# Kernel tuning notes

Hardware: AMD Instinct MI355X
Metric: run time of the kernel (lower is better)

## Reference

```python
import jax, jax.numpy as jnp
import numpy as np

HID, OUT, EMB, NL = 256, 128, 1024, 4
NR, NP_, NM = 16384, 40000, 30000
E = 200000
NTYPES = 3  # lin_nodes keys: protein, molecule, reaction


def setup_inputs() -> dict:
    key = jax.random.key(0)
    ks = jax.random.split(key, 32)
    f32 = jnp.float32
    inp = {}
    inp["x_reaction"] = jax.random.normal(ks[0], (NR, EMB), f32)
    inp["x_protein"] = jax.random.normal(ks[1], (NP_, EMB), f32)
    inp["x_molecule"] = jax.random.normal(ks[2], (NM, EMB), f32)
    inp["ei_p2r_src"] = jax.random.randint(ks[3], (E,), 0, NP_, jnp.int32)
    inp["ei_p2r_dst"] = jax.random.randint(ks[4], (E,), 0, NR, jnp.int32)
    inp["ei_m2r_src"] = jax.random.randint(ks[5], (E,), 0, NM, jnp.int32)
    inp["ei_m2r_dst"] = jax.random.randint(ks[6], (E,), 0, NR, jnp.int32)
    inp["ei_r2p_src"] = jax.random.randint(ks[7], (E,), 0, NR, jnp.int32)
    inp["ei_r2p_dst"] = jax.random.randint(ks[8], (E,), 0, NP_, jnp.int32)
    inp["ei_r2m_src"] = jax.random.randint(ks[9], (E,), 0, NR, jnp.int32)
    inp["ei_r2m_dst"] = jax.random.randint(ks[10], (E,), 0, NM, jnp.int32)
    inp["output_notes_opt"] = jax.random.normal(ks[11], (NR, EMB), f32)
    inp["output_types"] = jax.random.randint(ks[12], (NR,), 0, NTYPES, jnp.int32)
    s = 0.02
    # layer 0 SAGE params (lazy in_dim = EMB), one set per edge type (4 edge types)
    inp["Wl0"] = jax.random.normal(ks[13], (4, EMB, HID), f32) * s
    inp["Wr0"] = jax.random.normal(ks[14], (4, EMB, HID), f32) * s
    inp["bl0"] = jnp.zeros((4, HID), f32)
    # layers 1..3 SAGE params (in_dim = HID)
    inp["Wl"] = jax.random.normal(ks[15], (NL - 1, 4, HID, HID), f32) * s
    inp["Wr"] = jax.random.normal(ks[16], (NL - 1, 4, HID, HID), f32) * s
    inp["bl"] = jnp.zeros((NL - 1, 4, HID), f32)
    inp["W_reaction"] = jax.random.normal(ks[17], (HID, OUT), f32) * s
    inp["b_reaction"] = jnp.zeros((OUT,), f32)
    inp["W_nodes"] = jax.random.normal(ks[18], (NTYPES, EMB, OUT), f32) * s
    inp["b_nodes"] = jnp.zeros((NTYPES, OUT), f32)
    return inp


def _sage(x_src, x_dst, src, dst, n_dst, Wl, bl, Wr):
    # PyG SAGEConv (aggr='mean'): lin_l(mean_{j->i} x_j) + lin_r(x_i); lin_l has bias.
    g = x_src[src]                                              # [E, d] gather
    s = jax.ops.segment_sum(g, dst, num_segments=n_dst)          # [n_dst, d]
    cnt = jax.ops.segment_sum(jnp.ones((src.shape[0],), x_src.dtype), dst, num_segments=n_dst)
    mean = s / jnp.maximum(cnt, 1.0)[:, None]
    return mean @ Wl + bl + x_dst @ Wr


def _hetero_layer(xr, xp, xm, edges, Wl, bl, Wr):
    # HeteroConv(aggr='sum'): sum SAGE outputs per destination node type.
    (ps, pd), (ms, md), (rps, rpd), (rms, rmd) = edges
    new_r = (_sage(xp, xr, ps, pd, NR, Wl[0], bl[0], Wr[0])
             + _sage(xm, xr, ms, md, NR, Wl[1], bl[1], Wr[1]))
    new_p = _sage(xr, xp, rps, rpd, NP_, Wl[2], bl[2], Wr[2])
    new_m = _sage(xr, xm, rms, rmd, NM, Wl[3], bl[3], Wr[3])
    return new_r, new_p, new_m


def reference(x_reaction, x_protein, x_molecule,
              ei_p2r_src, ei_p2r_dst, ei_m2r_src, ei_m2r_dst,
              ei_r2p_src, ei_r2p_dst, ei_r2m_src, ei_r2m_dst,
              output_notes_opt, output_types,
              Wl0, bl0, Wr0, Wl, bl, Wr,
              W_reaction, b_reaction, W_nodes, b_nodes):
    edges = ((ei_p2r_src, ei_p2r_dst), (ei_m2r_src, ei_m2r_dst),
             (ei_r2p_src, ei_r2p_dst), (ei_r2m_src, ei_r2m_dst))
    xr, xp, xm = _hetero_layer(x_reaction, x_protein, x_molecule, edges, Wl0, bl0, Wr0)
    for l in range(NL - 1):
        xr, xp, xm = _hetero_layer(xr, xp, xm, edges, Wl[l], bl[l], Wr[l])
    reaction_out = xr @ W_reaction + b_reaction                  # [NR, OUT]
    # lin_nodes[t](v) per output node: project with all type linears, select by type id
    projs = jnp.einsum('ke,ted->ktd', output_notes_opt, W_nodes) + b_nodes[None]  # [NR, T, OUT]
    node_out = jnp.take_along_axis(projs, output_types[:, None, None].astype(jnp.int32), axis=1)[:, 0, :]
    # cosine similarity along dim=1, torch-style eps clamp on the norm product
    num = jnp.sum(reaction_out * node_out, axis=-1)
    den = jnp.maximum(jnp.linalg.norm(reaction_out, axis=-1) * jnp.linalg.norm(node_out, axis=-1), 1e-8)
    return (num / den + 1.0) * 0.5
```

## Files before the change

### kernel.cpp

```cpp
#include <hip/hip_runtime.h>
#include <math.h>
#include <stdint.h>

#define NR_ 16384
#define NP2_ 40000
#define NM_ 30000
#define NE_ 200000
#define EMB_ 1024
#define HID_ 256
#define OUTD_ 128

typedef __attribute__((ext_vector_type(8))) short bf16x8;
typedef __attribute__((ext_vector_type(4))) float f32x4;
typedef __attribute__((ext_vector_type(8))) unsigned short us8;

__device__ __forceinline__ unsigned short f2bf(float f) {
    uint32_t u = __builtin_bit_cast(uint32_t, f);
    u = (u + 0x7FFFu + ((u >> 16) & 1u)) >> 16;
    return (unsigned short)u;
}
__device__ __forceinline__ float bf2f(unsigned short u) {
    uint32_t v = ((uint32_t)u) << 16;
    return __builtin_bit_cast(float, v);
}

struct Csr4 {
    const int* src[4]; const int* dst[4];
    int* offs[4]; int* cur[4]; int* csr[4];
    int n[4];
};
__global__ void k_zero4(Csr4 c) {
    int y = blockIdx.y;
    int i = blockIdx.x * 256 + threadIdx.x;
    if (i < c.n[y]) c.cur[y][i] = 0;
}
__global__ void k_deg4(Csr4 c) {
    int y = blockIdx.y;
    int i = blockIdx.x * 256 + threadIdx.x;
    if (i < NE_) atomicAdd(&c.cur[y][c.dst[y][i]], 1);
}
__global__ void k_scanA(Csr4 c, int* __restrict__ csum) {
    int y = blockIdx.y;
    int n = c.n[y];
    int ch = blockIdx.x;
    int nch = (n + 1023) >> 10;
    if (ch >= nch) return;
    const int* deg = c.cur[y];
    int* offs = c.offs[y];
    __shared__ int ts[256];
    int base = ch << 10;
    int t = threadIdx.x;
    int v[4];
    int s = 0;
    #pragma unroll
    for (int k = 0; k < 4; ++k) {
        int i = base + t * 4 + k;
        v[k] = (i < n) ? deg[i] : 0;
        s += v[k];
    }
    ts[t] = s;
    __syncthreads();
    for (int st = 1; st < 256; st <<= 1) {
        int x = ts[t];
        int xo = (t >= st) ? ts[t - st] : 0;
        __syncthreads();
        ts[t] = x + xo;
        __syncthreads();
    }
    int run = (t > 0) ? ts[t - 1] : 0;
    #pragma unroll
    for (int k = 0; k < 4; ++k) {
        int i = base + t * 4 + k;
        if (i < n) offs[i] = run;
        run += v[k];
    }
    if (t == 255) csum[y * 40 + ch] = ts[255];
}
__global__ void k_scanB(Csr4 c, int* __restrict__ csum) {
    int y = threadIdx.x;
    if (y < 4) {
        int n = c.n[y];
        int nch = (n + 1023) >> 10;
        int acc = 0;
        for (int i = 0; i < nch; ++i) {
            int v = csum[y * 40 + i];
            csum[y * 40 + i] = acc;
            acc += v;
        }
        c.offs[y][n] = acc;
    }
}
__global__ void k_scanC(Csr4 c, const int* __restrict__ csum) {
    int y = blockIdx.y;
    int i = blockIdx.x * 256 + threadIdx.x;
    if (i < c.n[y]) {
        int v = c.offs[y][i] + csum[y * 40 + (i >> 10)];
        c.offs[y][i] = v;
        c.cur[y][i] = v;
    }
}
__global__ void k_scatter4(Csr4 c) {
    int y = blockIdx.y;
    int i = blockIdx.x * 256 + threadIdx.x;
    if (i < NE_) {
        int d = c.dst[y][i];
        int p = atomicAdd(&c.cur[y][d], 1);
        c.csr[y][p] = c.src[y][i];
    }
}

struct WItem { const float* a; const float* b; unsigned short* dst; int k; int n; };
struct WBatch { WItem it[32]; };
__global__ void k_wconvT(WBatch wb) {
    WItem w = wb.it[blockIdx.y];
    int total = w.k * w.n;
    int kmask = w.k - 1;
    int shift = (w.k == 1024) ? 10 : 8;
    for (int idx = blockIdx.x * 256 + threadIdx.x; idx < total; idx += gridDim.x * 256) {
        int k = idx & kmask, n = idx >> shift;
        float v = w.a[(size_t)k * w.n + n];
        if (w.b) v += w.b[(size_t)k * w.n + n];
        w.dst[idx] = f2bf(v);
    }
}

struct GSeg {
    const void* A; const unsigned short* Bt; void* C; const float* bias;
    int lda, ldc, M, K, ntn, blk0, af32;
};
struct GBatch { GSeg s[3]; int b1, b2, tot; };

template <bool OBF, bool AF32>
__global__ __launch_bounds__(256, 4) void k_gemmb(GBatch gb) {
    __shared__ __align__(16) unsigned short As[128 * 64];
    __shared__ __align__(16) unsigned short Bs[128 * 64];
    const int tid = threadIdx.x;
    const int lane = tid & 63;
    int nwg = gb.tot;
    int o = blockIdx.x;
    int q = nwg >> 3, r = nwg & 7;
    int xcd = o & 7, j = o >> 3;
    int wg = (xcd < r ? xcd * (q + 1) : r * (q + 1) + (xcd - r) * q) + j;
    const int si = (wg >= gb.b1) + (wg >= gb.b2);
    const GSeg sg = gb.s[si];
    const int local = wg - sg.blk0;
    const int bm = (local / sg.ntn) * 128;
    const int bn = (local % sg.ntn) * 128;
    const int lda = sg.lda, ldc = sg.ldc, M = sg.M, K = sg.K;
    const unsigned short* __restrict__ Bt = sg.Bt;
    const float* __restrict__ bias = sg.bias;

    const int wave = tid >> 6;
    const int wr = (wave >> 1) * 64;
    const int wc = (wave & 1) * 64;
    const int frow = lane & 15;
    const int fkc = lane >> 4;
    f32x4 acc[4][4] = {};

    for (int k0 = 0; k0 < K; k0 += 64) {
        #pragma unroll
        for (int i = 0; i < 4; ++i) {
            int c = tid + i * 256;
            int row = c >> 3, kc = c & 7;
            int srck = k0 + ((kc ^ (row & 7)) << 3);
            int ga = min(bm + row, M - 1);
            if constexpr (AF32) {
                const float* Af = (const float*)sg.A + (size_t)ga * lda + srck;
                float4 a0 = *(const float4*)Af;
                float4 a1 = *(const float4*)(Af + 4);
                us8 oo;
                oo[0] = f2bf(a0.x); oo[1] = f2bf(a0.y); oo[2] = f2bf(a0.z); oo[3] = f2bf(a0.w);
                oo[4] = f2bf(a1.x); oo[5] = f2bf(a1.y); oo[6] = f2bf(a1.z); oo[7] = f2bf(a1.w);
                *(us8*)(As + (size_t)c * 8) = oo;
            } else {
                __builtin_amdgcn_global_load_lds(
                    (const __attribute__((address_space(1))) unsigned int*)((const unsigned short*)sg.A + (size_t)ga * lda + srck),
                    (__attribute__((address_space(3))) unsigned int*)(As + (size_t)c * 8), 16, 0, 0);
            }
            __builtin_amdgcn_global_load_lds(
                (const __attribute__((address_space(1))) unsigned int*)(Bt + (size_t)(bn + row) * K + srck),
                (__attribute__((address_space(3))) unsigned int*)(Bs + (size_t)c * 8), 16, 0, 0);
        }
        __syncthreads();
        #pragma unroll
        for (int kk = 0; kk < 2; ++kk) {
            bf16x8 af[4], bfr[4];
            #pragma unroll
            for (int m = 0; m < 4; ++m) {
                int row = wr + m * 16 + frow;
                int kc = kk * 4 + fkc;
                af[m] = *(const bf16x8*)(As + (size_t)((row << 3) + (kc ^ (row & 7))) * 8);
            }
            #pragma unroll
            for (int n = 0; n < 4; ++n) {
                int row = wc + n * 16 + frow;
                int kc = kk * 4 + fkc;
                bfr[n] = *(const bf16x8*)(Bs + (size_t)((row << 3) + (kc ^ (row & 7))) * 8);
            }
            #pragma unroll
            for (int m = 0; m < 4; ++m)
                #pragma unroll
                for (int n = 0; n < 4; ++n)
                    acc[m][n] = __builtin_amdgcn_mfma_f32_16x16x32_bf16(bfr[n], af[m], acc[m][n], 0, 0, 0);
        }
        __syncthreads();
    }

    const int ccol0 = (lane >> 4) << 2;
    #pragma unroll
    for (int m = 0; m < 4; ++m) {
        int row = bm + wr + m * 16 + frow;
        if (row < M) {
            #pragma unroll
            for (int n = 0; n < 4; ++n) {
                int col = bn + wc + n * 16 + ccol0;
                f32x4 v = acc[m][n];
                if (bias) {
                    v[0] += bias[col + 0];
                    v[1] += bias[col + 1];
                    v[2] += bias[col + 2];
                    v[3] += bias[col + 3];
                }
                if constexpr (OBF) {
                    ushort4 oo;
                    oo.x = f2bf(v[0]); oo.y = f2bf(v[1]); oo.z = f2bf(v[2]); oo.w = f2bf(v[3]);
                    *(ushort4*)((unsigned short*)sg.C + (size_t)row * ldc + col) = oo;
                } else {
                    *(float4*)((float*)sg.C + (size_t)row * ldc + col) = make_float4(v[0], v[1], v[2], v[3]);
                }
            }
        }
    }
}

__global__ __launch_bounds__(256, 4) void k_gemmf(GBatch gb) {
    __shared__ __align__(16) unsigned short As[128 * 64];
    __shared__ __align__(16) unsigned short Bs[128 * 64];
    const int tid = threadIdx.x;
    const int lane = tid & 63;
    int nwg = gb.tot;
    int o = blockIdx.x;
    int q = nwg >> 3, r = nwg & 7;
    int xcd = o & 7, j = o >> 3;
    int wg = (xcd < r ? xcd * (q + 1) : r * (q + 1) + (xcd - r) * q) + j;
    const int si = (wg >= gb.b1) + (wg >= gb.b2);
    const GSeg sg = gb.s[si];
    const int local = wg - sg.blk0;
    const int bm = (local / sg.ntn) * 128;
    const int bn = (local % sg.ntn) * 128;
    const int lda = sg.lda, ldc = sg.ldc, M = sg.M, K = sg.K;
    const unsigned short* __restrict__ Bt = sg.Bt;
    const float* __restrict__ bias = sg.bias;

    const int wave = tid >> 6;
    const int wr = (wave >> 1) * 64;
    const int wc = (wave & 1) * 64;
    const int frow = lane & 15;
    const int fkc = lane >> 4;
    f32x4 acc[4][4] = {};

    for (int k0 = 0; k0 < K; k0 += 64) {
        #pragma unroll
        for (int i = 0; i < 4; ++i) {
            int c = tid + i * 256;
            int row = c >> 3, kc = c & 7;
            int srck = k0 + ((kc ^ (row & 7)) << 3);
            int ga = min(bm + row, M - 1);
            if (sg.af32) {
                const float* Af = (const float*)sg.A + (size_t)ga * lda + srck;
                float4 a0 = *(const float4*)Af;
                float4 a1 = *(const float4*)(Af + 4);
                us8 oo;
                oo[0] = f2bf(a0.x); oo[1] = f2bf(a0.y); oo[2] = f2bf(a0.z); oo[3] = f2bf(a0.w);
                oo[4] = f2bf(a1.x); oo[5] = f2bf(a1.y); oo[6] = f2bf(a1.z); oo[7] = f2bf(a1.w);
                *(us8*)(As + (size_t)c * 8) = oo;
            } else {
                __builtin_amdgcn_global_load_lds(
                    (const __attribute__((address_space(1))) unsigned int*)((const unsigned short*)sg.A + (size_t)ga * lda + srck),
                    (__attribute__((address_space(3))) unsigned int*)(As + (size_t)c * 8), 16, 0, 0);
            }
            __builtin_amdgcn_global_load_lds(
                (const __attribute__((address_space(1))) unsigned int*)(Bt + (size_t)(bn + row) * K + srck),
                (__attribute__((address_space(3))) unsigned int*)(Bs + (size_t)c * 8), 16, 0, 0);
        }
        __syncthreads();
        #pragma unroll
        for (int kk = 0; kk < 2; ++kk) {
            bf16x8 af[4], bfr[4];
            #pragma unroll
            for (int m = 0; m < 4; ++m) {
                int row = wr + m * 16 + frow;
                int kc = kk * 4 + fkc;
                af[m] = *(const bf16x8*)(As + (size_t)((row << 3) + (kc ^ (row & 7))) * 8);
            }
            #pragma unroll
            for (int n = 0; n < 4; ++n) {
                int row = wc + n * 16 + frow;
                int kc = kk * 4 + fkc;
                bfr[n] = *(const bf16x8*)(Bs + (size_t)((row << 3) + (kc ^ (row & 7))) * 8);
            }
            #pragma unroll
            for (int m = 0; m < 4; ++m)
                #pragma unroll
                for (int n = 0; n < 4; ++n)
                    acc[m][n] = __builtin_amdgcn_mfma_f32_16x16x32_bf16(bfr[n], af[m], acc[m][n], 0, 0, 0);
        }
        __syncthreads();
    }

    const int ccol0 = (lane >> 4) << 2;
    #pragma unroll
    for (int m = 0; m < 4; ++m) {
        int row = bm + wr + m * 16 + frow;
        if (row < M) {
            #pragma unroll
            for (int n = 0; n < 4; ++n) {
                int col = bn + wc + n * 16 + ccol0;
                f32x4 v = acc[m][n];
                v[0] += bias[col + 0];
                v[1] += bias[col + 1];
                v[2] += bias[col + 2];
                v[3] += bias[col + 3];
                *(float4*)((float*)sg.C + (size_t)row * ldc + col) = make_float4(v[0], v[1], v[2], v[3]);
            }
        }
    }
}

struct ASeg {
    const int* offsA; const int* csrA; const unsigned short* projA; int ldpA; const float* biasA;
    const int* offsB; const int* csrB; const unsigned short* projB; int ldpB; const float* biasB;
    unsigned short* outx; int ldo; int ndst; int blk0;
};
struct ABatch { ASeg s[3]; int b1, b2; };

__global__ __launch_bounds__(256) void k_aggb(ABatch ab) {
    int b = blockIdx.x;
    int si = (b >= ab.b1) + (b >= ab.b2);
    const ASeg sg = ab.s[si];
    int node = (b - sg.blk0) * 4 + (threadIdx.x >> 6);
    int lane = threadIdx.x & 63;
    if (node >= sg.ndst) return;

    float a0 = 0.f, a1 = 0.f, a2 = 0.f, a3 = 0.f;
    int begA = sg.offsA[node], endA = sg.offsA[node + 1];
    {
        const unsigned short* baseA = sg.projA + lane * 4;
        const int* csrA = sg.csrA;
        int ldpA = sg.ldpA;
        int e = begA;
        for (; e + 3 < endA; e += 4) {
            int i0 = csrA[e], i1 = csrA[e + 1], i2 = csrA[e + 2], i3 = csrA[e + 3];
            ushort4 u0 = *(const ushort4*)(baseA + (size_t)i0 * ldpA);
            ushort4 u1 = *(const ushort4*)(baseA + (size_t)i1 * ldpA);
            ushort4 u2 = *(const ushort4*)(baseA + (size_t)i2 * ldpA);
            ushort4 u3 = *(const ushort4*)(baseA + (size_t)i3 * ldpA);
            a0 += bf2f(u0.x) + bf2f(u1.x) + bf2f(u2.x) + bf2f(u3.x);
            a1 += bf2f(u0.y) + bf2f(u1.y) + bf2f(u2.y) + bf2f(u3.y);
            a2 += bf2f(u0.z) + bf2f(u1.z) + bf2f(u2.z) + bf2f(u3.z);
            a3 += bf2f(u0.w) + bf2f(u1.w) + bf2f(u2.w) + bf2f(u3.w);
        }
        for (; e < endA; ++e) {
            ushort4 u = *(const ushort4*)(baseA + (size_t)csrA[e] * ldpA);
            a0 += bf2f(u.x); a1 += bf2f(u.y); a2 += bf2f(u.z); a3 += bf2f(u.w);
        }
    }
    float invA = 1.f / fmaxf((float)(endA - begA), 1.f);
    float4 bA = ((const float4*)sg.biasA)[lane];
    float r0 = a0 * invA + bA.x;
    float r1 = a1 * invA + bA.y;
    float r2 = a2 * invA + bA.z;
    float r3 = a3 * invA + bA.w;

    if (sg.csrB) {
        float b0 = 0.f, b1 = 0.f, b2 = 0.f, b3 = 0.f;
        int begB = sg.offsB[node], endB = sg.offsB[node + 1];
        const unsigned short* baseB = sg.projB + lane * 4;
        const int* csrB = sg.csrB;
        int ldpB = sg.ldpB;
        int e = begB;
        for (; e + 3 < endB; e += 4) {
            int i0 = csrB[e], i1 = csrB[e + 1], i2 = csrB[e + 2], i3 = csrB[e + 3];
            ushort4 u0 = *(const ushort4*)(baseB + (size_t)i0 * ldpB);
            ushort4 u1 = *(const ushort4*)(baseB + (size_t)i1 * ldpB);
            ushort4 u2 = *(const ushort4*)(baseB + (size_t)i2 * ldpB);
            ushort4 u3 = *(const ushort4*)(baseB + (size_t)i3 * ldpB);
            b0 += bf2f(u0.x) + bf2f(u1.x) + bf2f(u2.x) + bf2f(u3.x);
            b1 += bf2f(u0.y) + bf2f(u1.y) + bf2f(u2.y) + bf2f(u3.y);
            b2 += bf2f(u0.z) + bf2f(u1.z) + bf2f(u2.z) + bf2f(u3.z);
            b3 += bf2f(u0.w) + bf2f(u1.w) + bf2f(u2.w) + bf2f(u3.w);
        }
        for (; e < endB; ++e) {
            ushort4 u = *(const ushort4*)(baseB + (size_t)csrB[e] * ldpB);
            b0 += bf2f(u.x); b1 += bf2f(u.y); b2 += bf2f(u.z); b3 += bf2f(u.w);
        }
        float invB = 1.f / fmaxf((float)(endB - begB), 1.f);
        float4 bB = ((const float4*)sg.biasB)[lane];
        r0 += b0 * invB + bB.x;
        r1 += b1 * invB + bB.y;
        r2 += b2 * invB + bB.z;
        r3 += b3 * invB + bB.w;
    }

    size_t o = (size_t)node * sg.ldo + lane * 4;
    ushort4 cur = *(const ushort4*)(sg.outx + o);
    ushort4 w;
    w.x = f2bf(bf2f(cur.x) + r0);
    w.y = f2bf(bf2f(cur.y) + r1);
    w.z = f2bf(bf2f(cur.z) + r2);
    w.w = f2bf(bf2f(cur.w) + r3);
    *(ushort4*)(sg.outx + o) = w;
}

__global__ __launch_bounds__(256) void k_cos(const float* __restrict__ ro,
                                             const float* __restrict__ pr,
                                             const int* __restrict__ types,
                                             float* __restrict__ out, int nr) {
    int row = blockIdx.x * 4 + (threadIdx.x >> 6);
    int lane = threadIdx.x & 63;
    if (row >= nr) return;
    int t = types[row];
    float2 r = ((const float2*)(ro + (size_t)row * OUTD_))[lane];
    float2 nn = ((const float2*)(pr + (size_t)row * 384 + t * OUTD_))[lane];
    float num = r.x * nn.x + r.y * nn.y;
    float d1 = r.x * r.x + r.y * r.y;
    float d2 = nn.x * nn.x + nn.y * nn.y;
    #pragma unroll
    for (int s = 1; s < 64; s <<= 1) {
        num += __shfl_xor(num, s);
        d1 += __shfl_xor(d1, s);
        d2 += __shfl_xor(d2, s);
    }
    if (lane == 0) out[row] = (num / fmaxf(sqrtf(d1) * sqrtf(d2), 1e-8f) + 1.f) * 0.5f;
}

extern "C" void kernel_launch(void* const* d_in, const int* in_sizes, int n_in,
                              void* d_out, int out_size, void* d_ws, size_t ws_size,
                              hipStream_t stream) {
    const float* x_r0 = (const float*)d_in[0];
    const float* x_p0 = (const float*)d_in[1];
    const float* x_m0 = (const float*)d_in[2];
    const int* e_src[4] = {(const int*)d_in[3], (const int*)d_in[5], (const int*)d_in[7], (const int*)d_in[9]};
    const int* e_dst[4] = {(const int*)d_in[4], (const int*)d_in[6], (const int*)d_in[8], (const int*)d_in[10]};
    const float* notes = (const float*)d_in[11];
    const int* types = (const int*)d_in[12];
    const float* Wl0 = (const float*)d_in[13];
    const float* Wr0 = (const float*)d_in[14];
    const float* bl0 = (const float*)d_in[15];
    const float* WlL = (const float*)d_in[16];
    const float* WrL = (const float*)d_in[17];
    const float* blL = (const float*)d_in[18];
    const float* Wre = (const float*)d_in[19];
    const float* bre = (const float*)d_in[20];
    const float* Wn  = (const float*)d_in[21];
    const float* bn  = (const float*)d_in[22];
    float* out = (float*)d_out;

    uintptr_t base = (uintptr_t)d_ws;
    auto alloc = [&](size_t bytes) -> void* {
        uintptr_t p = (base + 255) & ~(uintptr_t)255;
        base = p + bytes;
        return (void*)p;
    };
    unsigned short* Rb[2] = {(unsigned short*)alloc((size_t)NR_ * 768 * 2),
                             (unsigned short*)alloc((size_t)NR_ * 768 * 2)};
    unsigned short* Pb[2] = {(unsigned short*)alloc((size_t)NP2_ * 512 * 2),
                             (unsigned short*)alloc((size_t)NP2_ * 512 * 2)};
    unsigned short* Mb[2] = {(unsigned short*)alloc((size_t)NM_ * 512 * 2),
                             (unsigned short*)alloc((size_t)NM_ * 512 * 2)};
    float* ro = (float*)alloc((size_t)NR_ * OUTD_ * 4);
    float* pr = (float*)alloc((size_t)NR_ * 384 * 4);
    unsigned short* wbf = (unsigned short*)alloc((size_t)4000000 * 2);
    int* csum = (int*)alloc(160 * 4);
    int nd[4] = {NR_, NR_, NP2_, NM_};
    Csr4 cs{};
    for (int t = 0; t < 4; ++t) {
        cs.src[t] = e_src[t]; cs.dst[t] = e_dst[t]; cs.n[t] = nd[t];
        cs.offs[t] = (int*)alloc(((size_t)nd[t] + 1) * 4);
        cs.cur[t]  = (int*)alloc((size_t)nd[t] * 4);
        cs.csr[t]  = (int*)alloc((size_t)NE_ * 4);
    }

    unsigned short *BR[4], *BP[4], *BM[4], *Bre, *Bn;
    {
        WBatch wb{};
        int cnt = 0;
        size_t woff = 0;
        auto add = [&](const float* a, const float* bb, int K, int N) -> unsigned short* {
            unsigned short* dst = wbf + woff;
            woff += (size_t)K * N;
            wb.it[cnt] = WItem{a, bb, dst, K, N};
            ++cnt;
            return dst;
        };
        const size_t w0 = (size_t)EMB_ * HID_;
        const size_t wl = (size_t)HID_ * HID_;
        for (int l = 0; l < 4; ++l) {
            int K = (l == 0) ? EMB_ : HID_;
            const float* Wr_ = (l == 0) ? Wr0 : WrL + (size_t)(l - 1) * 4 * wl;
            const float* Wl_ = (l == 0) ? Wl0 : WlL + (size_t)(l - 1) * 4 * wl;
            size_t ws_ = (l == 0) ? w0 : wl;
            BR[l] = add(Wr_ + 0 * ws_, Wr_ + 1 * ws_, K, HID_);
            add(Wl_ + 2 * ws_, nullptr, K, HID_);
            add(Wl_ + 3 * ws_, nullptr, K, HID_);
            BP[l] = add(Wr_ + 2 * ws_, nullptr, K, HID_);
            add(Wl_ + 0 * ws_, nullptr, K, HID_);
            BM[l] = add(Wr_ + 3 * ws_, nullptr, K, HID_);
            add(Wl_ + 1 * ws_, nullptr, K, HID_);
        }
        Bre = add(Wre, nullptr, HID_, OUTD_);
        Bn = add(Wn + 0 * (size_t)EMB_ * OUTD_, nullptr, EMB_, OUTD_);
        add(Wn + 1 * (size_t)EMB_ * OUTD_, nullptr, EMB_, OUTD_);
        add(Wn + 2 * (size_t)EMB_ * OUTD_, nullptr, EMB_, OUTD_);
        k_wconvT<<<dim3(128, cnt), 256, 0, stream>>>(wb);
    }

    k_zero4<<<dim3((NP2_ + 255) / 256, 4), 256, 0, stream>>>(cs);
    k_deg4<<<dim3((NE_ + 255) / 256, 4), 256, 0, stream>>>(cs);
    k_scanA<<<dim3(40, 4), 256, 0, stream>>>(cs, csum);
    k_scanB<<<1, 64, 0, stream>>>(cs, csum);
    k_scanC<<<dim3((NP2_ + 255) / 256, 4), 256, 0, stream>>>(cs, csum);
    k_scatter4<<<dim3((NE_ + 255) / 256, 4), 256, 0, stream>>>(cs);

    const int MT_R = (NR_ + 127) / 128;
    const int MT_P = (NP2_ + 127) / 128;
    const int MT_M = (NM_ + 127) / 128;
    auto seg = [](const void* A, const unsigned short* Bt, void* C, const float* bias,
                  int lda, int ldc, int M, int K, int ntn, int blk0, int af32) -> GSeg {
        return GSeg{A, Bt, C, bias, lda, ldc, M, K, ntn, blk0, af32};
    };

    const int AB_R = (NR_ + 3) / 4, AB_P = (NP2_ + 3) / 4, AB_M = (NM_ + 3) / 4;

    for (int l = 0; l < 4; ++l) {
        int K = (l == 0) ? EMB_ : HID_;
        unsigned short* R = Rb[l & 1];
        unsigned short* P = Pb[l & 1];
        unsigned short* M = Mb[l & 1];
        const float* bl_ = (l == 0) ? bl0 : blL + (size_t)(l - 1) * 4 * HID_;

        GBatch gb{};
        int nR = MT_R * 6, nP = MT_P * 4, nM = MT_M * 4;
        if (l == 0) {
            gb.s[0] = seg(x_r0, BR[0], R, nullptr, EMB_, 768, NR_, EMB_, 6, 0, 1);
            gb.s[1] = seg(x_p0, BP[0], P, nullptr, EMB_, 512, NP2_, EMB_, 4, nR, 1);
            gb.s[2] = seg(x_m0, BM[0], M, nullptr, EMB_, 512, NM_, EMB_, 4, nR + nP, 1);
        } else {
            gb.s[0] = seg(Rb[(l - 1) & 1], BR[l], R, nullptr, 768, 768, NR_, K, 6, 0, 0);
            gb.s[1] = seg(Pb[(l - 1) & 1], BP[l], P, nullptr, 512, 512, NP2_, K, 4, nR, 0);
            gb.s[2] = seg(Mb[(l - 1) & 1], BM[l], M, nullptr, 512, 512, NM_, K, 4, nR + nP, 0);
        }
        gb.b1 = nR; gb.b2 = nR + nP; gb.tot = nR + nP + nM;
        if (l == 0) k_gemmb<true, true><<<gb.tot, 256, 0, stream>>>(gb);
        else        k_gemmb<true, false><<<gb.tot, 256, 0, stream>>>(gb);

        ABatch ab{};
        ab.s[0] = ASeg{cs.offs[0], cs.csr[0], P + 256, 512, bl_ + 0 * HID_,
                       cs.offs[1], cs.csr[1], M + 256, 512, bl_ + 1 * HID_,
                       R, 768, NR_, 0};
        ab.s[1] = ASeg{cs.offs[2], cs.csr[2], R + 256, 768, bl_ + 2 * HID_,
                       nullptr, nullptr, nullptr, 0, nullptr,
                       P, 512, NP2_, AB_R};
        ab.s[2] = ASeg{cs.offs[3], cs.csr[3], R + 512, 768, bl_ + 3 * HID_,
                       nullptr, nullptr, nullptr, 0, nullptr,
                       M, 512, NM_, AB_R + AB_P};
        ab.b1 = AB_R; ab.b2 = AB_R + AB_P;
        k_aggb<<<AB_R + AB_P + AB_M, 256, 0, stream>>>(ab);
    }

    {
        GBatch gf{};
        gf.s[0] = seg(Rb[1], Bre, ro, bre, 768, OUTD_, NR_, HID_, 1, 0, 0);
        gf.s[1] = seg(notes, Bn, pr, bn, EMB_, 384, NR_, EMB_, 3, MT_R, 1);
        gf.s[2] = gf.s[1];
        gf.b1 = MT_R; gf.b2 = MT_R + MT_R * 3; gf.tot = MT_R + MT_R * 3;
        k_gemmf<<<gf.tot, 256, 0, stream>>>(gf);
    }
    k_cos<<<NR_ / 4, 256, 0, stream>>>(ro, pr, types, out, NR_);
}
```

Before: 834.2 us.

## Add register-prefetch double-buffered GEMM for fp32-A inputs and split final GEMMs

Adds a new GEMM kernel for fp32 A operands that prefetches the next A tile into registers and double-buffers the B tile in shared memory, so global load latency overlaps with MFMA compute. It is used for the layer-0 and node-projection GEMMs. The mixed final GEMM is split into two launches (a bf16-A one and an fp32-A one), which removes the runtime af32 branch. Launch bounds drop from 4 to 3 waves per SIMD to leave room for the extra registers and LDS, at the cost of lower occupancy.

```diff
diff --git a/kernel.cpp b/kernel.cpp
--- a/kernel.cpp
+++ b/kernel.cpp
@@ -126,12 +126,12 @@
 
 struct GSeg {
     const void* A; const unsigned short* Bt; void* C; const float* bias;
-    int lda, ldc, M, K, ntn, blk0, af32;
+    int lda, ldc, M, K, ntn, blk0;
 };
 struct GBatch { GSeg s[3]; int b1, b2, tot; };
 
-template <bool OBF, bool AF32>
-__global__ __launch_bounds__(256, 4) void k_gemmb(GBatch gb) {
+template <bool OBF>
+__global__ __launch_bounds__(256, 3) void k_gemmb(GBatch gb) {
     __shared__ __align__(16) unsigned short As[128 * 64];
     __shared__ __align__(16) unsigned short Bs[128 * 64];
     const int tid = threadIdx.x;
@@ -164,19 +164,9 @@
             int row = c >> 3, kc = c & 7;
             int srck = k0 + ((kc ^ (row & 7)) << 3);
             int ga = min(bm + row, M - 1);
-            if constexpr (AF32) {
-                const float* Af = (const float*)sg.A + (size_t)ga * lda + srck;
-                float4 a0 = *(const float4*)Af;
-                float4 a1 = *(const float4*)(Af + 4);
-                us8 oo;
-                oo[0] = f2bf(a0.x); oo[1] = f2bf(a0.y); oo[2] = f2bf(a0.z); oo[3] = f2bf(a0.w);
-                oo[4] = f2bf(a1.x); oo[5] = f2bf(a1.y); oo[6] = f2bf(a1.z); oo[7] = f2bf(a1.w);
-                *(us8*)(As + (size_t)c * 8) = oo;
-            } else {
-                __builtin_amdgcn_global_load_lds(
-                    (const __attribute__((address_space(1))) unsigned int*)((const unsigned short*)sg.A + (size_t)ga * lda + srck),
-                    (__attribute__((address_space(3))) unsigned int*)(As + (size_t)c * 8), 16, 0, 0);
-            }
+            __builtin_amdgcn_global_load_lds(
+                (const __attribute__((address_space(1))) unsigned int*)((const unsigned short*)sg.A + (size_t)ga * lda + srck),
+                (__attribute__((address_space(3))) unsigned int*)(As + (size_t)c * 8), 16, 0, 0);
             __builtin_amdgcn_global_load_lds(
                 (const __attribute__((address_space(1))) unsigned int*)(Bt + (size_t)(bn + row) * K + srck),
                 (__attribute__((address_space(3))) unsigned int*)(Bs + (size_t)c * 8), 16, 0, 0);
@@ -233,9 +223,10 @@
     }
 }
 
-__global__ __launch_bounds__(256, 4) void k_gemmf(GBatch gb) {
+template <bool OBF>
+__global__ __launch_bounds__(256, 3) void k_gemma(GBatch gb) {
     __shared__ __align__(16) unsigned short As[128 * 64];
-    __shared__ __align__(16) unsigned short Bs[128 * 64];
+    __shared__ __align__(16) unsigned short Bs[2][128 * 64];
     const int tid = threadIdx.x;
     const int lane = tid & 63;
     int nwg = gb.tot;
@@ -258,55 +249,83 @@
     const int frow = lane & 15;
     const int fkc = lane >> 4;
     f32x4 acc[4][4] = {};
-
-    for (int k0 = 0; k0 < K; k0 += 64) {
-        #pragma unroll
-        for (int i = 0; i < 4; ++i) {
-            int c = tid + i * 256;
-            int row = c >> 3, kc = c & 7;
-            int srck = k0 + ((kc ^ (row & 7)) << 3);
-            int ga = min(bm + row, M - 1);
-            if (sg.af32) {
-                const float* Af = (const float*)sg.A + (size_t)ga * lda + srck;
-                float4 a0 = *(const float4*)Af;
-                float4 a1 = *(const float4*)(Af + 4);
-                us8 oo;
-                oo[0] = f2bf(a0.x); oo[1] = f2bf(a0.y); oo[2] = f2bf(a0.z); oo[3] = f2bf(a0.w);
-                oo[4] = f2bf(a1.x); oo[5] = f2bf(a1.y); oo[6] = f2bf(a1.z); oo[7] = f2bf(a1.w);
-                *(us8*)(As + (size_t)c * 8) = oo;
-            } else {
-                __builtin_amdgcn_global_load_lds(
-                    (const __attribute__((address_space(1))) unsigned int*)((const unsigned short*)sg.A + (size_t)ga * lda + srck),
-                    (__attribute__((address_space(3))) unsigned int*)(As + (size_t)c * 8), 16, 0, 0);
-            }
-            __builtin_amdgcn_global_load_lds(
-                (const __attribute__((address_space(1))) unsigned int*)(Bt + (size_t)(bn + row) * K + srck),
-                (__attribute__((address_space(3))) unsigned int*)(Bs + (size_t)c * 8), 16, 0, 0);
-        }
+    float4 ra0[4], ra1[4];
+
+#define ALOAD(kk0) do {                                                                    \
+    _Pragma("unroll")                                                                      \
+    for (int i = 0; i < 4; ++i) {                                                          \
+        int c = tid + i * 256, rw = c >> 3, kc = c & 7;                                    \
+        int srck = (kk0) + ((kc ^ (rw & 7)) << 3);                                         \
+        int ga = min(bm + rw, M - 1);                                                      \
+        const float* Af = (const float*)sg.A + (size_t)ga * lda + srck;                    \
+        ra0[i] = *(const float4*)Af;                                                       \
+        ra1[i] = *(const float4*)(Af + 4);                                                 \
+    } } while (0)
+
+#define AWRITE() do {                                                                      \
+    _Pragma("unroll")                                                                      \
+    for (int i = 0; i < 4; ++i) {                                                          \
+        int c = tid + i * 256;                                                             \
+        us8 oo;                                                                            \
+        oo[0] = f2bf(ra0[i].x); oo[1] = f2bf(ra0[i].y);                                    \
+        oo[2] = f2bf(ra0[i].z); oo[3] = f2bf(ra0[i].w);                                    \
+        oo[4] = f2bf(ra1[i].x); oo[5] = f2bf(ra1[i].y);                                    \
+        oo[6] = f2bf(ra1[i].z); oo[7] = f2bf(ra1[i].w);                                    \
+        *(us8*)(As + (size_t)c * 8) = oo;                                                  \
+    } } while (0)
+
+#define STAGE_B(bufi, kk0) do {                                                            \
+    _Pragma("unroll")                                                                      \
+    for (int i = 0; i < 4; ++i) {                                                          \
+        int c = tid + i * 256, rw = c >> 3, kc = c & 7;                                    \
+        int srck = (kk0) + ((kc ^ (rw & 7)) << 3);                                         \
+        __builtin_amdgcn_global_load_lds(                                                  \
+            (const __attribute__((address_space(1))) unsigned int*)(Bt + (size_t)(bn + rw) * K + srck), \
+            (__attribute__((address_space(3))) unsigned int*)(&Bs[bufi][(size_t)c * 8]), 16, 0, 0); \
+    } } while (0)
+
+#define COMPUTE(bufi) do {                                                                 \
+    _Pragma("unroll")                                                                      \
+    for (int kk = 0; kk < 2; ++kk) {                                                       \
+        bf16x8 af[4], bfr[4];                                                              \
+        _Pragma("unroll")                                                                  \
+        for (int m = 0; m < 4; ++m) {                                                      \
+            int rw = wr + m * 16 + frow;                                                   \
+            int kc = kk * 4 + fkc;                                                         \
+            af[m] = *(const bf16x8*)(As + (size_t)((rw << 3) + (kc ^ (rw & 7))) * 8);      \
+        }                                                                                  \
+        _Pragma("unroll")                                                                  \
+        for (int n = 0; n < 4; ++n) {                                                      \
+            int rw = wc + n * 16 + frow;                                                   \
+            int kc = kk * 4 + fkc;                                                         \
+            bfr[n] = *(const bf16x8*)(&Bs[bufi][(size_t)((rw << 3) + (kc ^ (rw & 7))) * 8]); \
+        }                                                                                  \
+        _Pragma("unroll")                                                                  \
+        for (int m = 0; m < 4; ++m)                                                        \
+            _Pragma("unroll")                                                              \
+            for (int n = 0; n < 4; ++n)                                                    \
+                acc[m][n] = __builtin_amdgcn_mfma_f32_16x16x32_bf16(bfr[n], af[m], acc[m][n], 0, 0, 0); \
+    } } while (0)
+
+    const int nt = K >> 6;
+    ALOAD(0);
+    STAGE_B(0, 0);
+    AWRITE();
+    __syncthreads();
+    for (int t = 0; t < nt; ++t) {
+        if (t + 1 < nt) {
+            ALOAD((t + 1) << 6);
+            STAGE_B((t + 1) & 1, (t + 1) << 6);
+        }
+        COMPUTE(t & 1);
         __syncthreads();
-        #pragma unroll
-        for (int kk = 0; kk < 2; ++kk) {
-            bf16x8 af[4], bfr[4];
-            #pragma unroll
-            for (int m = 0; m < 4; ++m) {
-                int row = wr + m * 16 + frow;
-                int kc = kk * 4 + fkc;
-                af[m] = *(const bf16x8*)(As + (size_t)((row << 3) + (kc ^ (row & 7))) * 8);
-            }
-            #pragma unroll
-            for (int n = 0; n < 4; ++n) {
-                int row = wc + n * 16 + frow;
-                int kc = kk * 4 + fkc;
-                bfr[n] = *(const bf16x8*)(Bs + (size_t)((row << 3) + (kc ^ (row & 7))) * 8);
-            }
-            #pragma unroll
-            for (int m = 0; m < 4; ++m)
-                #pragma unroll
-                for (int n = 0; n < 4; ++n)
-                    acc[m][n] = __builtin_amdgcn_mfma_f32_16x16x32_bf16(bfr[n], af[m], acc[m][n], 0, 0, 0);
-        }
+        if (t + 1 < nt) AWRITE();
         __syncthreads();
     }
+#undef ALOAD
+#undef AWRITE
+#undef STAGE_B
+#undef COMPUTE
 
     const int ccol0 = (lane >> 4) << 2;
     #pragma unroll
@@ -317,11 +336,19 @@
             for (int n = 0; n < 4; ++n) {
                 int col = bn + wc + n * 16 + ccol0;
                 f32x4 v = acc[m][n];
-                v[0] += bias[col + 0];
-                v[1] += bias[col + 1];
-                v[2] += bias[col + 2];
-                v[3] += bias[col + 3];
-                *(float4*)((float*)sg.C + (size_t)row * ldc + col) = make_float4(v[0], v[1], v[2], v[3]);
+                if (bias) {
+                    v[0] += bias[col + 0];
+                    v[1] += bias[col + 1];
+                    v[2] += bias[col + 2];
+                    v[3] += bias[col + 3];
+                }
+                if constexpr (OBF) {
+                    ushort4 oo;
+                    oo.x = f2bf(v[0]); oo.y = f2bf(v[1]); oo.z = f2bf(v[2]); oo.w = f2bf(v[3]);
+                    *(ushort4*)((unsigned short*)sg.C + (size_t)row * ldc + col) = oo;
+                } else {
+                    *(float4*)((float*)sg.C + (size_t)row * ldc + col) = make_float4(v[0], v[1], v[2], v[3]);
+                }
             }
         }
     }
@@ -526,8 +553,8 @@
     const int MT_P = (NP2_ + 127) / 128;
     const int MT_M = (NM_ + 127) / 128;
     auto seg = [](const void* A, const unsigned short* Bt, void* C, const float* bias,
-                  int lda, int ldc, int M, int K, int ntn, int blk0, int af32) -> GSeg {
-        return GSeg{A, Bt, C, bias, lda, ldc, M, K, ntn, blk0, af32};
+                  int lda, int ldc, int M, int K, int ntn, int blk0) -> GSeg {
+        return GSeg{A, Bt, C, bias, lda, ldc, M, K, ntn, blk0};
     };
 
     const int AB_R = (NR_ + 3) / 4, AB_P = (NP2_ + 3) / 4, AB_M = (NM_ + 3) / 4;
@@ -542,17 +569,17 @@
         GBatch gb{};
         int nR = MT_R * 6, nP = MT_P * 4, nM = MT_M * 4;
         if (l == 0) {
-            gb.s[0] = seg(x_r0, BR[0], R, nullptr, EMB_, 768, NR_, EMB_, 6, 0, 1);
-            gb.s[1] = seg(x_p0, BP[0], P, nullptr, EMB_, 512, NP2_, EMB_, 4, nR, 1);
-            gb.s[2] = seg(x_m0, BM[0], M, nullptr, EMB_, 512, NM_, EMB_, 4, nR + nP, 1);
+            gb.s[0] = seg(x_r0, BR[0], R, nullptr, EMB_, 768, NR_, EMB_, 6, 0);
+            gb.s[1] = seg(x_p0, BP[0], P, nullptr, EMB_, 512, NP2_, EMB_, 4, nR);
+            gb.s[2] = seg(x_m0, BM[0], M, nullptr, EMB_, 512, NM_, EMB_, 4, nR + nP);
         } else {
-            gb.s[0] = seg(Rb[(l - 1) & 1], BR[l], R, nullptr, 768, 768, NR_, K, 6, 0, 0);
-            gb.s[1] = seg(Pb[(l - 1) & 1], BP[l], P, nullptr, 512, 512, NP2_, K, 4, nR, 0);
-            gb.s[2] = seg(Mb[(l - 1) & 1], BM[l], M, nullptr, 512, 512, NM_, K, 4, nR + nP, 0);
+            gb.s[0] = seg(Rb[(l - 1) & 1], BR[l], R, nullptr, 768, 768, NR_, K, 6, 0);
+            gb.s[1] = seg(Pb[(l - 1) & 1], BP[l], P, nullptr, 512, 512, NP2_, K, 4, nR);
+            gb.s[2] = seg(Mb[(l - 1) & 1], BM[l], M, nullptr, 512, 512, NM_, K, 4, nR + nP);
         }
         gb.b1 = nR; gb.b2 = nR + nP; gb.tot = nR + nP + nM;
-        if (l == 0) k_gemmb<true, true><<<gb.tot, 256, 0, stream>>>(gb);
-        else        k_gemmb<true, false><<<gb.tot, 256, 0, stream>>>(gb);
+        if (l == 0) k_gemma<true><<<gb.tot, 256, 0, stream>>>(gb);
+        else        k_gemmb<true><<<gb.tot, 256, 0, stream>>>(gb);
 
         ABatch ab{};
         ab.s[0] = ASeg{cs.offs[0], cs.csr[0], P + 256, 512, bl_ + 0 * HID_,
@@ -569,12 +596,14 @@
     }
 
     {
-        GBatch gf{};
-        gf.s[0] = seg(Rb[1], Bre, ro, bre, 768, OUTD_, NR_, HID_, 1, 0, 0);
-        gf.s[1] = seg(notes, Bn, pr, bn, EMB_, 384, NR_, EMB_, 3, MT_R, 1);
-        gf.s[2] = gf.s[1];
-        gf.b1 = MT_R; gf.b2 = MT_R + MT_R * 3; gf.tot = MT_R + MT_R * 3;
-        k_gemmf<<<gf.tot, 256, 0, stream>>>(gf);
+        GBatch g1{};
+        g1.s[0] = seg(Rb[1], Bre, ro, bre, 768, OUTD_, NR_, HID_, 1, 0);
+        g1.b1 = g1.b2 = g1.tot = MT_R;
+        k_gemmb<false><<<g1.tot, 256, 0, stream>>>(g1);
+        GBatch g2{};
+        g2.s[0] = seg(notes, Bn, pr, bn, EMB_, 384, NR_, EMB_, 3, 0);
+        g2.b1 = g2.b2 = g2.tot = MT_R * 3;
+        k_gemma<false><<<g2.tot, 256, 0, stream>>>(g2);
     }
     k_cos<<<NR_ / 4, 256, 0, stream>>>(ro, pr, types, out, NR_);
 }
```

Measured after the change: 782.5 us. 6.2% less time.

## Enlarge GEMM tiles to 256x128 with 512-thread blocks and split final GEMM

Applied to the files above, without the earlier changes.

The batched GEMM kernel now computes 256-row by 128-column tiles using 512 threads (8 waves), doubling the A tile in LDS while sharing each B tile across twice as many rows. This cuts redundant loads of the weight tiles and halves the number of workgroups. The separate final-projection kernel is removed; the final projections now run as two launches of the templated kernel with compile-time A-format flags instead of a runtime branch. In exchange LDS use per block grows, which may lower occupancy, and the bigger tiles waste more work on partial tiles at the row edges.

```diff
diff --git a/kernel.cpp b/kernel.cpp
--- a/kernel.cpp
+++ b/kernel.cpp
@@ -126,13 +126,13 @@
 
 struct GSeg {
     const void* A; const unsigned short* Bt; void* C; const float* bias;
-    int lda, ldc, M, K, ntn, blk0, af32;
+    int lda, ldc, M, K, ntn, blk0;
 };
 struct GBatch { GSeg s[3]; int b1, b2, tot; };
 
 template <bool OBF, bool AF32>
-__global__ __launch_bounds__(256, 4) void k_gemmb(GBatch gb) {
-    __shared__ __align__(16) unsigned short As[128 * 64];
+__global__ __launch_bounds__(512, 6) void k_gemmb(GBatch gb) {
+    __shared__ __align__(16) unsigned short As[256 * 64];
     __shared__ __align__(16) unsigned short Bs[128 * 64];
     const int tid = threadIdx.x;
     const int lane = tid & 63;
@@ -144,7 +144,7 @@
     const int si = (wg >= gb.b1) + (wg >= gb.b2);
     const GSeg sg = gb.s[si];
     const int local = wg - sg.blk0;
-    const int bm = (local / sg.ntn) * 128;
+    const int bm = (local / sg.ntn) * 256;
     const int bn = (local % sg.ntn) * 128;
     const int lda = sg.lda, ldc = sg.ldc, M = sg.M, K = sg.K;
     const unsigned short* __restrict__ Bt = sg.Bt;
@@ -160,7 +160,7 @@
     for (int k0 = 0; k0 < K; k0 += 64) {
         #pragma unroll
         for (int i = 0; i < 4; ++i) {
-            int c = tid + i * 256;
+            int c = tid + i * 512;
             int row = c >> 3, kc = c & 7;
             int srck = k0 + ((kc ^ (row & 7)) << 3);
             int ga = min(bm + row, M - 1);
@@ -177,6 +177,12 @@
                     (const __attribute__((address_space(1))) unsigned int*)((const unsigned short*)sg.A + (size_t)ga * lda + srck),
                     (__attribute__((address_space(3))) unsigned int*)(As + (size_t)c * 8), 16, 0, 0);
             }
+        }
+        #pragma unroll
+        for (int i = 0; i < 2; ++i) {
+            int c = tid + i * 512;
+            int row = c >> 3, kc = c & 7;
+            int srck = k0 + ((kc ^ (row & 7)) << 3);
             __builtin_amdgcn_global_load_lds(
                 (const __attribute__((address_space(1))) unsigned int*)(Bt + (size_t)(bn + row) * K + srck),
                 (__attribute__((address_space(3))) unsigned int*)(Bs + (size_t)c * 8), 16, 0, 0);
@@ -228,100 +234,6 @@
                 } else {
                     *(float4*)((float*)sg.C + (size_t)row * ldc + col) = make_float4(v[0], v[1], v[2], v[3]);
                 }
-            }
-        }
-    }
-}
-
-__global__ __launch_bounds__(256, 4) void k_gemmf(GBatch gb) {
-    __shared__ __align__(16) unsigned short As[128 * 64];
-    __shared__ __align__(16) unsigned short Bs[128 * 64];
-    const int tid = threadIdx.x;
-    const int lane = tid & 63;
-    int nwg = gb.tot;
-    int o = blockIdx.x;
-    int q = nwg >> 3, r = nwg & 7;
-    int xcd = o & 7, j = o >> 3;
-    int wg = (xcd < r ? xcd * (q + 1) : r * (q + 1) + (xcd - r) * q) + j;
-    const int si = (wg >= gb.b1) + (wg >= gb.b2);
-    const GSeg sg = gb.s[si];
-    const int local = wg - sg.blk0;
-    const int bm = (local / sg.ntn) * 128;
-    const int bn = (local % sg.ntn) * 128;
-    const int lda = sg.lda, ldc = sg.ldc, M = sg.M, K = sg.K;
-    const unsigned short* __restrict__ Bt = sg.Bt;
-    const float* __restrict__ bias = sg.bias;
-
-    const int wave = tid >> 6;
-    const int wr = (wave >> 1) * 64;
-    const int wc = (wave & 1) * 64;
-    const int frow = lane & 15;
-    const int fkc = lane >> 4;
-    f32x4 acc[4][4] = {};
-
-    for (int k0 = 0; k0 < K; k0 += 64) {
-        #pragma unroll
-        for (int i = 0; i < 4; ++i) {
-            int c = tid + i * 256;
-            int row = c >> 3, kc = c & 7;
-            int srck = k0 + ((kc ^ (row & 7)) << 3);
-            int ga = min(bm + row, M - 1);
-            if (sg.af32) {
-                const float* Af = (const float*)sg.A + (size_t)ga * lda + srck;
-                float4 a0 = *(const float4*)Af;
-                float4 a1 = *(const float4*)(Af + 4);
-                us8 oo;
-                oo[0] = f2bf(a0.x); oo[1] = f2bf(a0.y); oo[2] = f2bf(a0.z); oo[3] = f2bf(a0.w);
-                oo[4] = f2bf(a1.x); oo[5] = f2bf(a1.y); oo[6] = f2bf(a1.z); oo[7] = f2bf(a1.w);
-                *(us8*)(As + (size_t)c * 8) = oo;
-            } else {
-                __builtin_amdgcn_global_load_lds(
-                    (const __attribute__((address_space(1))) unsigned int*)((const unsigned short*)sg.A + (size_t)ga * lda + srck),
-                    (__attribute__((address_space(3))) unsigned int*)(As + (size_t)c * 8), 16, 0, 0);
-            }
-            __builtin_amdgcn_global_load_lds(
-                (const __attribute__((address_space(1))) unsigned int*)(Bt + (size_t)(bn + row) * K + srck),
-                (__attribute__((address_space(3))) unsigned int*)(Bs + (size_t)c * 8), 16, 0, 0);
-        }
-        __syncthreads();
-        #pragma unroll
-        for (int kk = 0; kk < 2; ++kk) {
-            bf16x8 af[4], bfr[4];
-            #pragma unroll
-            for (int m = 0; m < 4; ++m) {
-                int row = wr + m * 16 + frow;
-                int kc = kk * 4 + fkc;
-                af[m] = *(const bf16x8*)(As + (size_t)((row << 3) + (kc ^ (row & 7))) * 8);
-            }
-            #pragma unroll
-            for (int n = 0; n < 4; ++n) {
-                int row = wc + n * 16 + frow;
-                int kc = kk * 4 + fkc;
-                bfr[n] = *(const bf16x8*)(Bs + (size_t)((row << 3) + (kc ^ (row & 7))) * 8);
-            }
-            #pragma unroll
-            for (int m = 0; m < 4; ++m)
-                #pragma unroll
-                for (int n = 0; n < 4; ++n)
-                    acc[m][n] = __builtin_amdgcn_mfma_f32_16x16x32_bf16(bfr[n], af[m], acc[m][n], 0, 0, 0);
-        }
-        __syncthreads();
-    }
-
-    const int ccol0 = (lane >> 4) << 2;
-    #pragma unroll
-    for (int m = 0; m < 4; ++m) {
-        int row = bm + wr + m * 16 + frow;
-        if (row < M) {
-            #pragma unroll
-            for (int n = 0; n < 4; ++n) {
-                int col = bn + wc + n * 16 + ccol0;
-                f32x4 v = acc[m][n];
-                v[0] += bias[col + 0];
-                v[1] += bias[col + 1];
-                v[2] += bias[col + 2];
-                v[3] += bias[col + 3];
-                *(float4*)((float*)sg.C + (size_t)row * ldc + col) = make_float4(v[0], v[1], v[2], v[3]);
             }
         }
     }
@@ -522,12 +434,12 @@
     k_scanC<<<dim3((NP2_ + 255) / 256, 4), 256, 0, stream>>>(cs, csum);
     k_scatter4<<<dim3((NE_ + 255) / 256, 4), 256, 0, stream>>>(cs);
 
-    const int MT_R = (NR_ + 127) / 128;
-    const int MT_P = (NP2_ + 127) / 128;
-    const int MT_M = (NM_ + 127) / 128;
+    const int MT_R = (NR_ + 255) / 256;
+    const int MT_P = (NP2_ + 255) / 256;
+    const int MT_M = (NM_ + 255) / 256;
     auto seg = [](const void* A, const unsigned short* Bt, void* C, const float* bias,
-                  int lda, int ldc, int M, int K, int ntn, int blk0, int af32) -> GSeg {
-        return GSeg{A, Bt, C, bias, lda, ldc, M, K, ntn, blk0, af32};
+                  int lda, int ldc, int M, int K, int ntn, int blk0) -> GSeg {
+        return GSeg{A, Bt, C, bias, lda, ldc, M, K, ntn, blk0};
     };
 
     const int AB_R = (NR_ + 3) / 4, AB_P = (NP2_ + 3) / 4, AB_M = (NM_ + 3) / 4;
@@ -542,17 +454,17 @@
         GBatch gb{};
         int nR = MT_R * 6, nP = MT_P * 4, nM = MT_M * 4;
         if (l == 0) {
-            gb.s[0] = seg(x_r0, BR[0], R, nullptr, EMB_, 768, NR_, EMB_, 6, 0, 1);
-            gb.s[1] = seg(x_p0, BP[0], P, nullptr, EMB_, 512, NP2_, EMB_, 4, nR, 1);
-            gb.s[2] = seg(x_m0, BM[0], M, nullptr, EMB_, 512, NM_, EMB_, 4, nR + nP, 1);
+            gb.s[0] = seg(x_r0, BR[0], R, nullptr, EMB_, 768, NR_, EMB_, 6, 0);
+            gb.s[1] = seg(x_p0, BP[0], P, nullptr, EMB_, 512, NP2_, EMB_, 4, nR);
+            gb.s[2] = seg(x_m0, BM[0], M, nullptr, EMB_, 512, NM_, EMB_, 4, nR + nP);
         } else {
-            gb.s[0] = seg(Rb[(l - 1) & 1], BR[l], R, nullptr, 768, 768, NR_, K, 6, 0, 0);
-            gb.s[1] = seg(Pb[(l - 1) & 1], BP[l], P, nullptr, 512, 512, NP2_, K, 4, nR, 0);
-            gb.s[2] = seg(Mb[(l - 1) & 1], BM[l], M, nullptr, 512, 512, NM_, K, 4, nR + nP, 0);
+            gb.s[0] = seg(Rb[(l - 1) & 1], BR[l], R, nullptr, 768, 768, NR_, K, 6, 0);
+            gb.s[1] = seg(Pb[(l - 1) & 1], BP[l], P, nullptr, 512, 512, NP2_, K, 4, nR);
+            gb.s[2] = seg(Mb[(l - 1) & 1], BM[l], M, nullptr, 512, 512, NM_, K, 4, nR + nP);
         }
         gb.b1 = nR; gb.b2 = nR + nP; gb.tot = nR + nP + nM;
-        if (l == 0) k_gemmb<true, true><<<gb.tot, 256, 0, stream>>>(gb);
-        else        k_gemmb<true, false><<<gb.tot, 256, 0, stream>>>(gb);
+        if (l == 0) k_gemmb<true, true><<<gb.tot, 512, 0, stream>>>(gb);
+        else        k_gemmb<true, false><<<gb.tot, 512, 0, stream>>>(gb);
 
         ABatch ab{};
         ab.s[0] = ASeg{cs.offs[0], cs.csr[0], P + 256, 512, bl_ + 0 * HID_,
@@ -569,12 +481,14 @@
     }
 
     {
-        GBatch gf{};
-        gf.s[0] = seg(Rb[1], Bre, ro, bre, 768, OUTD_, NR_, HID_, 1, 0, 0);
-        gf.s[1] = seg(notes, Bn, pr, bn, EMB_, 384, NR_, EMB_, 3, MT_R, 1);
-        gf.s[2] = gf.s[1];
-        gf.b1 = MT_R; gf.b2 = MT_R + MT_R * 3; gf.tot = MT_R + MT_R * 3;
-        k_gemmf<<<gf.tot, 256, 0, stream>>>(gf);
+        GBatch g1{};
+        g1.s[0] = seg(Rb[1], Bre, ro, bre, 768, OUTD_, NR_, HID_, 1, 0);
+        g1.b1 = g1.b2 = g1.tot = MT_R;
+        k_gemmb<false, false><<<g1.tot, 512, 0, stream>>>(g1);
+        GBatch g2{};
+        g2.s[0] = seg(notes, Bn, pr, bn, EMB_, 384, NR_, EMB_, 3, 0);
+        g2.b1 = g2.b2 = g2.tot = MT_R * 3;
+        k_gemmb<false, true><<<g2.tot, 512, 0, stream>>>(g2);
     }
     k_cos<<<NR_ / 4, 256, 0, stream>>>(ro, pr, types, out, NR_);
 }
```

Measured after the change: 2.201 ms. +163.8%, slower.
